# Kernel tuning notes

Measured on AMD Instinct MI355X. Metric: run time of the kernel, lower is better.

The kernel has to match this reference:

```python
import jax, jax.numpy as jnp
import numpy as np

EPSILON = 1e-8
K = 3  # three-nearest-neighbor interpolation


def setup_inputs() -> dict:
    key = jax.random.key(0)
    k1, k2, k3 = jax.random.split(key, 3)
    B, N1, N2, C = 8, 1024, 4096, 256
    p1 = jax.random.normal(k1, (B, N1, 3), dtype=jnp.float32)  # coarse coords
    x1 = jax.random.normal(k2, (B, C, N1), dtype=jnp.float32)  # coarse features (channel-first)
    p2 = jax.random.normal(k3, (B, N2, 3), dtype=jnp.float32)  # fine coords
    return {"p1": p1, "x1": x1, "p2": p2}


def reference(p1, x1, p2):
    # Squared pairwise distances [B, N2, N1] via the expansion trick.
    d2 = (
        jnp.sum(p2 * p2, axis=-1, keepdims=True)
        - 2.0 * jnp.einsum("bmd,bnd->bmn", p2, p1)
        + jnp.sum(p1 * p1, axis=-1)[:, None, :]
    )
    # K smallest distances (pointops.nearestneighbor returns squared dists).
    neg_top, idx = jax.lax.top_k(-d2, K)  # [B, N2, K]
    dist = -neg_top
    # Reciprocal-distance weights, normalized over the K neighbors.
    dist_recip = 1.0 / (dist + EPSILON)
    weight = dist_recip / jnp.sum(dist_recip, axis=-1, keepdims=True)  # [B, N2, K]
    # Gather neighbor features and blend: up_x1[b,c,m] = sum_k w[b,m,k] * x1[b,c,idx[b,m,k]]
    x1t = jnp.swapaxes(x1, 1, 2)  # [B, N1, C]
    gathered = jax.vmap(lambda f, i: f[i])(x1t, idx)  # [B, N2, K, C]
    up_x1 = jnp.einsum("bmkc,bmk->bcm", gathered, weight)  # [B, C, N2]
    return up_x1
```

## Files before the change

kernel.cpp:

```cpp
#include <hip/hip_runtime.h>
#include <cfloat>
#include <climits>

#define B_   8
#define N1_  1024
#define N2_  4096
#define C_   256
#define TPQ  16
#define QPB  (256 / TPQ)


__device__ __forceinline__ bool better_(float d, int i, float D, int I) {
    return (d < D) || (d == D && i < I);
}

__device__ __forceinline__ void ins_(float d, int i,
                                     float& d0, float& d1, float& d2,
                                     int& i0, int& i1, int& i2) {
    if (better_(d, i, d2, i2)) {
        d2 = d; i2 = i;
        if (better_(d2, i2, d1, i1)) {
            float td = d1; d1 = d2; d2 = td;
            int   ti = i1; i1 = i2; i2 = ti;
            if (better_(d1, i1, d0, i0)) {
                td = d0; d0 = d1; d1 = td;
                ti = i0; i0 = i1; i1 = ti;
            }
        }
    }
}

__global__ __launch_bounds__(256) void knn_kernel(
    const float* __restrict__ p1, const float* __restrict__ p2,
    int4* __restrict__ wsi, float4* __restrict__ wsw) {
    __shared__ float4 pts[N1_];

    const int tid   = threadIdx.x;
    const int b     = blockIdx.x >> 8;
    const int mtile = blockIdx.x & 255;

    for (int j = tid; j < N1_; j += 256) {
        float x = p1[((size_t)b * N1_ + j) * 3 + 0];
        float y = p1[((size_t)b * N1_ + j) * 3 + 1];
        float z = p1[((size_t)b * N1_ + j) * 3 + 2];
        float s1 = __fadd_rn(__fadd_rn(__fmul_rn(x, x), __fmul_rn(y, y)),
                             __fmul_rn(z, z));
        pts[j] = make_float4(x + x, y + y, z + z, s1);
    }
    __syncthreads();

    const int q = tid >> 4;
    const int t = tid & 15;
    const int m = mtile * QPB + q;

    const size_t pbase = ((size_t)b * N2_ + m) * 3;
    const float x2 = p2[pbase + 0];
    const float y2 = p2[pbase + 1];
    const float z2 = p2[pbase + 2];
    const float s2 = __fadd_rn(__fadd_rn(__fmul_rn(x2, x2), __fmul_rn(y2, y2)),
                               __fmul_rn(z2, z2));

    float d0 = FLT_MAX, d1 = FLT_MAX, d2 = FLT_MAX;
    int   i0 = INT_MAX, i1 = INT_MAX, i2 = INT_MAX;

#pragma unroll 4
    for (int n = t; n < N1_; n += TPQ) {
        float4 p = pts[n];
        float dot2 = __fadd_rn(__fadd_rn(__fmul_rn(x2, p.x), __fmul_rn(y2, p.y)),
                               __fmul_rn(z2, p.z));
        float dd = __fadd_rn(__fsub_rn(s2, dot2), p.w);

        bool c0 = dd < d0;
        bool c1 = dd < d1;
        bool c2 = dd < d2;
        float n0 = fminf(dd, d0);
        float n1 = __builtin_amdgcn_fmed3f(dd, d0, d1);
        float n2 = __builtin_amdgcn_fmed3f(dd, d1, d2);
        int j0 = c0 ? n : i0;
        int j1 = c1 ? (c0 ? i0 : n) : i1;
        int j2 = c2 ? (c1 ? i1 : n) : i2;
        d0 = n0; d1 = n1; d2 = n2;
        i0 = j0; i1 = j1; i2 = j2;
    }

    for (int mask = 1; mask < TPQ; mask <<= 1) {
        float pd0 = __shfl_xor(d0, mask, TPQ);
        float pd1 = __shfl_xor(d1, mask, TPQ);
        float pd2 = __shfl_xor(d2, mask, TPQ);
        int   pi0 = __shfl_xor(i0, mask, TPQ);
        int   pi1 = __shfl_xor(i1, mask, TPQ);
        int   pi2 = __shfl_xor(i2, mask, TPQ);
        ins_(pd0, pi0, d0, d1, d2, i0, i1, i2);
        ins_(pd1, pi1, d0, d1, d2, i0, i1, i2);
        ins_(pd2, pi2, d0, d1, d2, i0, i1, i2);
    }

    if (t == 0) {
        float r0 = 1.0f / __fadd_rn(d0, 1e-8f);
        float r1 = 1.0f / __fadd_rn(d1, 1e-8f);
        float r2 = 1.0f / __fadd_rn(d2, 1e-8f);
        float s  = __fadd_rn(__fadd_rn(r0, r1), r2);
        const size_t o = (size_t)b * N2_ + m;
        wsi[o] = make_int4(i0, i1, i2, 0);
        wsw[o] = make_float4(r0 / s, r1 / s, r2 / s, 0.0f);
    }
}


__global__ __launch_bounds__(256) void blend_kernel(
    const float* __restrict__ x1, const int4* __restrict__ wsi,
    const float4* __restrict__ wsw, float* __restrict__ out) {
    __shared__ float L[4][N1_];

    int bid = blockIdx.x;
    const int mhalf = bid & 1;
    const int ct    = (bid >> 1) & 63;
    const int b     = bid >> 7;
    const int tid   = threadIdx.x;

    const float* src = x1 + ((size_t)b * C_ + ct * 4) * N1_;
    float4* Lv = reinterpret_cast<float4*>(&L[0][0]);
    const float4* Sv = reinterpret_cast<const float4*>(src);
#pragma unroll
    for (int j = 0; j < 4; ++j) Lv[tid + 256 * j] = Sv[tid + 256 * j];
    __syncthreads();

    const size_t wbase = (size_t)b * N2_;
    const size_t obase = ((size_t)b * C_ + (size_t)ct * 4) * N2_;

#pragma unroll
    for (int mb = 0; mb < 8; ++mb) {
        const int m = mhalf * 2048 + mb * 256 + tid;
        const int4   id = wsi[wbase + m];
        const float4 w  = wsw[wbase + m];
#pragma unroll
        for (int r = 0; r < 4; ++r) {
            float a  = L[r][id.x];
            float bb = L[r][id.y];
            float cc = L[r][id.z];
            float acc = __fadd_rn(__fadd_rn(__fmul_rn(a,  w.x),
                                            __fmul_rn(bb, w.y)),
                                  __fmul_rn(cc, w.z));
            __builtin_nontemporal_store(acc, &out[obase + (size_t)r * N2_ + m]);
        }
    }
}

extern "C" void kernel_launch(void* const* d_in, const int* in_sizes, int n_in,
                              void* d_out, int out_size, void* d_ws, size_t ws_size,
                              hipStream_t stream) {
    const float* p1 = (const float*)d_in[0];
    const float* x1 = (const float*)d_in[1];
    const float* p2 = (const float*)d_in[2];
    float* out = (float*)d_out;

    int4*   wsi = (int4*)d_ws;
    float4* wsw = (float4*)((char*)d_ws + (size_t)B_ * N2_ * sizeof(int4));

    knn_kernel<<<B_ * (N2_ / QPB), 256, 0, stream>>>(p1, p2, wsi, wsw);
    blend_kernel<<<B_ * (C_ / 4) * 2, 256, 0, stream>>>(x1, wsi, wsw, out);
}
```

Baseline: 33.09 us.

## Pack coarse points in pairs for packed-FP32 distance math in KNN scan

Stores the coarse points in shared memory as split-pair SoA arrays (x,y pairs in one float4, z and squared-norm pairs in another) so each thread computes two candidate distances with two-wide float vectors that can map to packed FP32 instructions. Each thread now scans adjacent point pairs instead of strided singles, and the cross-lane merge is rewritten as branch-free selects. The goal is to halve the ALU cost of distance evaluation and remove divergent branches in the reduction. Fp contraction is disabled to keep rounding identical to the reference, and the order in which candidates are scanned changes, so tie handling depends on the lexicographic merge.

```diff
diff --git a/kernel.cpp b/kernel.cpp
--- a/kernel.cpp
+++ b/kernel.cpp
@@ -9,43 +9,63 @@
 #define TPQ  16
 #define QPB  (256 / TPQ)
 
+typedef float vf2 __attribute__((ext_vector_type(2)));
 
-__device__ __forceinline__ bool better_(float d, int i, float D, int I) {
-    return (d < D) || (d == D && i < I);
+
+__device__ __forceinline__ void ins_lex_(float pd, int pi,
+                                         float& d0, float& d1, float& d2,
+                                         int& i0, int& i1, int& i2) {
+    bool l0 = (pd < d0) || (pd == d0 && pi < i0);
+    bool l1 = (pd < d1) || (pd == d1 && pi < i1);
+    bool l2 = (pd < d2) || (pd == d2 && pi < i2);
+    float e0 = l0 ? pd : d0;
+    float e1 = l1 ? (l0 ? d0 : pd) : d1;
+    float e2 = l2 ? (l1 ? d1 : pd) : d2;
+    int   f0 = l0 ? pi : i0;
+    int   f1 = l1 ? (l0 ? i0 : pi) : i1;
+    int   f2 = l2 ? (l1 ? i1 : pi) : i2;
+    d0 = e0; d1 = e1; d2 = e2; i0 = f0; i1 = f1; i2 = f2;
 }
 
-__device__ __forceinline__ void ins_(float d, int i,
-                                     float& d0, float& d1, float& d2,
-                                     int& i0, int& i1, int& i2) {
-    if (better_(d, i, d2, i2)) {
-        d2 = d; i2 = i;
-        if (better_(d2, i2, d1, i1)) {
-            float td = d1; d1 = d2; d2 = td;
-            int   ti = i1; i1 = i2; i2 = ti;
-            if (better_(d1, i1, d0, i0)) {
-                td = d0; d0 = d1; d1 = td;
-                ti = i0; i0 = i1; i1 = ti;
-            }
-        }
-    }
+__device__ __forceinline__ void ins_scan_(float dd, int n,
+                                          float& d0, float& d1, float& d2,
+                                          int& i0, int& i1, int& i2) {
+    bool c0 = dd < d0;
+    bool c1 = dd < d1;
+    bool c2 = dd < d2;
+    float n0 = fminf(dd, d0);
+    float n1 = __builtin_amdgcn_fmed3f(dd, d0, d1);
+    float n2 = __builtin_amdgcn_fmed3f(dd, d1, d2);
+    int ta = c0 ? i0 : n;
+    int j0 = c0 ? n  : i0;
+    int j1 = c1 ? ta : i1;
+    int tb = c1 ? i1 : n;
+    int j2 = c2 ? tb : i2;
+    d0 = n0; d1 = n1; d2 = n2;
+    i0 = j0; i1 = j1; i2 = j2;
 }
 
 __global__ __launch_bounds__(256) void knn_kernel(
     const float* __restrict__ p1, const float* __restrict__ p2,
     int4* __restrict__ wsi, float4* __restrict__ wsw) {
-    __shared__ float4 pts[N1_];
+#pragma clang fp contract(off)
+    __shared__ float4 Q[N1_ / 2];
+    __shared__ float4 R[N1_ / 2];
 
     const int tid   = threadIdx.x;
     const int b     = blockIdx.x >> 8;
     const int mtile = blockIdx.x & 255;
 
-    for (int j = tid; j < N1_; j += 256) {
-        float x = p1[((size_t)b * N1_ + j) * 3 + 0];
-        float y = p1[((size_t)b * N1_ + j) * 3 + 1];
-        float z = p1[((size_t)b * N1_ + j) * 3 + 2];
-        float s1 = __fadd_rn(__fadd_rn(__fmul_rn(x, x), __fmul_rn(y, y)),
-                             __fmul_rn(z, z));
-        pts[j] = make_float4(x + x, y + y, z + z, s1);
+    for (int k = tid; k < N1_ / 2; k += 256) {
+        const float* pa = &p1[((size_t)b * N1_ + 2 * k) * 3];
+        float xa = pa[0], ya = pa[1], za = pa[2];
+        float xb = pa[3], yb = pa[4], zb = pa[5];
+        float sa = __fadd_rn(__fadd_rn(__fmul_rn(xa, xa), __fmul_rn(ya, ya)),
+                             __fmul_rn(za, za));
+        float sb = __fadd_rn(__fadd_rn(__fmul_rn(xb, xb), __fmul_rn(yb, yb)),
+                             __fmul_rn(zb, zb));
+        Q[k] = make_float4(xa + xa, xb + xb, ya + ya, yb + yb);
+        R[k] = make_float4(za + za, zb + zb, sa, sb);
     }
     __syncthreads();
 
@@ -60,27 +80,30 @@
     const float s2 = __fadd_rn(__fadd_rn(__fmul_rn(x2, x2), __fmul_rn(y2, y2)),
                                __fmul_rn(z2, z2));
 
+    const vf2 x2v = {x2, x2};
+    const vf2 y2v = {y2, y2};
+    const vf2 z2v = {z2, z2};
+    const vf2 s2v = {s2, s2};
+
     float d0 = FLT_MAX, d1 = FLT_MAX, d2 = FLT_MAX;
     int   i0 = INT_MAX, i1 = INT_MAX, i2 = INT_MAX;
 
 #pragma unroll 4
-    for (int n = t; n < N1_; n += TPQ) {
-        float4 p = pts[n];
-        float dot2 = __fadd_rn(__fadd_rn(__fmul_rn(x2, p.x), __fmul_rn(y2, p.y)),
-                               __fmul_rn(z2, p.z));
-        float dd = __fadd_rn(__fsub_rn(s2, dot2), p.w);
-
-        bool c0 = dd < d0;
-        bool c1 = dd < d1;
-        bool c2 = dd < d2;
-        float n0 = fminf(dd, d0);
-        float n1 = __builtin_amdgcn_fmed3f(dd, d0, d1);
-        float n2 = __builtin_amdgcn_fmed3f(dd, d1, d2);
-        int j0 = c0 ? n : i0;
-        int j1 = c1 ? (c0 ? i0 : n) : i1;
-        int j2 = c2 ? (c1 ? i1 : n) : i2;
-        d0 = n0; d1 = n1; d2 = n2;
-        i0 = j0; i1 = j1; i2 = j2;
+    for (int j = 0; j < N1_ / (2 * TPQ); ++j) {
+        const int k = t + TPQ * j;
+        float4 qv = Q[k];
+        float4 rv = R[k];
+        vf2 qx = {qv.x, qv.y};
+        vf2 qy = {qv.z, qv.w};
+        vf2 rz = {rv.x, rv.y};
+        vf2 rs = {rv.z, rv.w};
+        vf2 t1 = qx * x2v;
+        vf2 t2 = qy * y2v;
+        vf2 t3 = rz * z2v;
+        vf2 dot2 = (t1 + t2) + t3;
+        vf2 dd = (s2v - dot2) + rs;
+        ins_scan_(dd.x, 2 * k,     d0, d1, d2, i0, i1, i2);
+        ins_scan_(dd.y, 2 * k + 1, d0, d1, d2, i0, i1, i2);
     }
 
     for (int mask = 1; mask < TPQ; mask <<= 1) {
@@ -90,9 +113,9 @@
         int   pi0 = __shfl_xor(i0, mask, TPQ);
         int   pi1 = __shfl_xor(i1, mask, TPQ);
         int   pi2 = __shfl_xor(i2, mask, TPQ);
-        ins_(pd0, pi0, d0, d1, d2, i0, i1, i2);
-        ins_(pd1, pi1, d0, d1, d2, i0, i1, i2);
-        ins_(pd2, pi2, d0, d1, d2, i0, i1, i2);
+        ins_lex_(pd0, pi0, d0, d1, d2, i0, i1, i2);
+        ins_lex_(pd1, pi1, d0, d1, d2, i0, i1, i2);
+        ins_lex_(pd2, pi2, d0, d1, d2, i0, i1, i2);
     }
 
     if (t == 0) {
```

New measurement: 34.71 us. 4.9% more time.

## Transpose blend tile to channel-interleaved float4 LDS with XOR swizzle, prefetch indices

Applied to the files above, without the earlier changes.

The blend kernel now stores the four-channel feature tile in LDS as one float4 per source point, XOR-swizzled, so each neighbor gather is a single 128-bit LDS read instead of four scalar reads. All eight index/weight records per thread are loaded into registers before the tile is staged, so their global latency overlaps the x1 load and the barrier. The cost is more registers per thread and an in-register transpose plus swizzled LDS writes during staging.

```diff
diff --git a/kernel.cpp b/kernel.cpp
--- a/kernel.cpp
+++ b/kernel.cpp
@@ -110,7 +110,7 @@
 __global__ __launch_bounds__(256) void blend_kernel(
     const float* __restrict__ x1, const int4* __restrict__ wsi,
     const float4* __restrict__ wsw, float* __restrict__ out) {
-    __shared__ float L[4][N1_];
+    __shared__ float4 L4[N1_];
 
     int bid = blockIdx.x;
     const int mhalf = bid & 1;
@@ -118,29 +118,42 @@
     const int b     = bid >> 7;
     const int tid   = threadIdx.x;
 
-    const float* src = x1 + ((size_t)b * C_ + ct * 4) * N1_;
-    float4* Lv = reinterpret_cast<float4*>(&L[0][0]);
-    const float4* Sv = reinterpret_cast<const float4*>(src);
+    const size_t wbase = (size_t)b * N2_ + (size_t)mhalf * 2048;
+    int4   id[8];
+    float4 w[8];
 #pragma unroll
-    for (int j = 0; j < 4; ++j) Lv[tid + 256 * j] = Sv[tid + 256 * j];
+    for (int mb = 0; mb < 8; ++mb) {
+        id[mb] = wsi[wbase + mb * 256 + tid];
+        w[mb]  = wsw[wbase + mb * 256 + tid];
+    }
+
+    const float* src = x1 + ((size_t)b * C_ + (size_t)ct * 4) * N1_;
+    float4 v[4];
+#pragma unroll
+    for (int c = 0; c < 4; ++c)
+        v[c] = reinterpret_cast<const float4*>(src + (size_t)c * N1_)[tid];
+#pragma unroll
+    for (int e = 0; e < 4; ++e) {
+        const int n = 4 * tid + e;
+        L4[n ^ ((n >> 3) & 7)] = make_float4((&v[0].x)[e], (&v[1].x)[e],
+                                             (&v[2].x)[e], (&v[3].x)[e]);
+    }
     __syncthreads();
 
-    const size_t wbase = (size_t)b * N2_;
     const size_t obase = ((size_t)b * C_ + (size_t)ct * 4) * N2_;
-
 #pragma unroll
     for (int mb = 0; mb < 8; ++mb) {
         const int m = mhalf * 2048 + mb * 256 + tid;
-        const int4   id = wsi[wbase + m];
-        const float4 w  = wsw[wbase + m];
+        const int na = id[mb].x, nb = id[mb].y, nc = id[mb].z;
+        const float4 A  = L4[na ^ ((na >> 3) & 7)];
+        const float4 Bv = L4[nb ^ ((nb >> 3) & 7)];
+        const float4 Cv = L4[nc ^ ((nc >> 3) & 7)];
+        const float wx = w[mb].x, wy = w[mb].y, wz = w[mb].z;
 #pragma unroll
         for (int r = 0; r < 4; ++r) {
-            float a  = L[r][id.x];
-            float bb = L[r][id.y];
-            float cc = L[r][id.z];
-            float acc = __fadd_rn(__fadd_rn(__fmul_rn(a,  w.x),
-                                            __fmul_rn(bb, w.y)),
-                                  __fmul_rn(cc, w.z));
+            float acc = __fadd_rn(__fadd_rn(__fmul_rn((&A.x)[r],  wx),
+                                            __fmul_rn((&Bv.x)[r], wy)),
+                                  __fmul_rn((&Cv.x)[r], wz));
             __builtin_nontemporal_store(acc, &out[obase + (size_t)r * N2_ + m]);
         }
     }
```

Result: no change. 33.07 us (-0.1%).
